# Performance work log

Measured on AMD Instinct MI355X. Metric: run time of the kernel, lower is better.

Reference implementation:

```python
import jax, jax.numpy as jnp
import numpy as np
from jax import lax

EPS = 1e-12  # F.normalize eps


def _normalize(x, axis):
    n = jnp.linalg.norm(x, axis=axis, keepdims=True)
    return x / jnp.maximum(n, EPS)


def setup_inputs() -> dict:
    key = jax.random.key(0)
    k1, k2 = jax.random.split(key)
    B, T, C, E = 4, 4096, 2048, 64
    return {
        "hidden_states": jax.random.normal(k1, (B, T, C), dtype=jnp.float32),
        "sim_matrix": jax.random.normal(k2, (C, E), dtype=jnp.float32),
        "gates": jnp.zeros((E,), dtype=jnp.float32),
        "temperature": jnp.ones((1,), dtype=jnp.float32),
        "experts_mask": jnp.ones((E,), dtype=jnp.float32),
        "min_experts_per_tok": 2,
    }


def reference(hidden_states, sim_matrix, gates, temperature, experts_mask, min_experts_per_tok):
    B, T, C = hidden_states.shape
    E = sim_matrix.shape[1]
    flat = hidden_states.reshape(B * T, C)  # (N, C)

    logit_scale = jax.nn.sigmoid(temperature)[0]
    # cosine-similarity style gating: row-normalized tokens x col-normalized sim matrix
    logits = _normalize(flat, axis=-1) @ _normalize(sim_matrix, axis=0)  # (N, E)
    logits = logits * experts_mask

    gated = jax.nn.relu(logits - gates * logit_scale)  # (N, E)
    hard = (gated > 0).astype(gated.dtype)
    # STE: forward = hard threshold, backward = identity on gated
    ste_mask = gated + lax.stop_gradient(hard - gated)

    # fallback: rows with no active expert get top-k(min_experts_per_tok) of logits
    inactive = jnp.sum(hard, axis=1) == 0  # (N,)
    _, topk_idx = lax.top_k(logits, min_experts_per_tok)  # (N, k)
    fallback = jnp.sum(jax.nn.one_hot(topk_idx, E, dtype=gated.dtype), axis=1)  # (N, E)

    activation_mask = jnp.where(inactive[:, None], fallback, ste_mask)
    return activation_mask, logits
```

## Files before the change

kernel.cpp:

```cpp
#include <hip/hip_runtime.h>
#include <cstdint>
#include <math.h>

#define N_TOK 16384
#define C_DIM 2048
#define E_DIM 64
#define TILE_T 64
#define KC 64
#define EPSN 1e-12f
#define NE ((size_t)N_TOK * E_DIM)

#define SCRATCH_FAST (6 * N_TOK * E_DIM + C_DIM * E_DIM + N_TOK + E_DIM)
#define SCRATCH_OLD (C_DIM * E_DIM + N_TOK + E_DIM)

__global__ __launch_bounds__(1024) void coln_kernel(const float* __restrict__ sim,
                                                    float* __restrict__ denc) {
    __shared__ float S[2][256 * 64];
    const int tid = threadIdx.x;
    {
        const float4* src = (const float4*)sim;
        float4* dst = (float4*)S[0];
        for (int i = tid; i < 4096; i += 1024) dst[i] = src[i];
    }
    __syncthreads();
    float acc = 0.f;
    for (int ch = 0; ch < 8; ++ch) {
        if (ch + 1 < 8) {
            const float4* src = (const float4*)(sim + (size_t)(ch + 1) * 256 * 64);
            float4* dst = (float4*)S[(ch + 1) & 1];
            for (int i = tid; i < 4096; i += 1024) dst[i] = src[i];
        }
        if (tid < 64) {
            const float* Sc = S[ch & 1];
#pragma unroll 8
            for (int r = 0; r < 256; ++r) {
                const float v = Sc[r * 64 + tid];
                acc = __fadd_rn(acc, __fmul_rn(v, v));
            }
        }
        __syncthreads();
    }
    if (tid < 64) denc[tid] = fmaxf(__fsqrt_rn(acc), EPSN);
}

__global__ __launch_bounds__(256) void bn_kernel(const float* __restrict__ sim,
                                                 const float* __restrict__ denc,
                                                 float* __restrict__ bnorm) {
    const int idx = blockIdx.x * 256 + threadIdx.x;
    const int e = idx & (E_DIM - 1);
    bnorm[idx] = __fdiv_rn(sim[idx], denc[e]);
}

__global__ __launch_bounds__(256) void tokn_kernel(const float* __restrict__ hs,
                                                   float* __restrict__ ntok) {
    const int t = blockIdx.x * 16 + (threadIdx.x >> 4);
    const int j = threadIdx.x & 15;
    const float4* p = (const float4*)(hs + (size_t)t * C_DIM + j * 128);
    float4 v0 = p[0], v1 = p[1];
    float r0 = __fmul_rn(v0.x, v0.x), r1 = __fmul_rn(v0.y, v0.y);
    float r2 = __fmul_rn(v0.z, v0.z), r3 = __fmul_rn(v0.w, v0.w);
    float r4 = __fmul_rn(v1.x, v1.x), r5 = __fmul_rn(v1.y, v1.y);
    float r6 = __fmul_rn(v1.z, v1.z), r7 = __fmul_rn(v1.w, v1.w);
#pragma unroll
    for (int i = 2; i < 32; i += 2) {
        float4 a = p[i], b = p[i + 1];
        r0 = __fadd_rn(r0, __fmul_rn(a.x, a.x));
        r1 = __fadd_rn(r1, __fmul_rn(a.y, a.y));
        r2 = __fadd_rn(r2, __fmul_rn(a.z, a.z));
        r3 = __fadd_rn(r3, __fmul_rn(a.w, a.w));
        r4 = __fadd_rn(r4, __fmul_rn(b.x, b.x));
        r5 = __fadd_rn(r5, __fmul_rn(b.y, b.y));
        r6 = __fadd_rn(r6, __fmul_rn(b.z, b.z));
        r7 = __fadd_rn(r7, __fmul_rn(b.w, b.w));
    }
    float leaf = __fadd_rn(__fadd_rn(__fadd_rn(r0, r1), __fadd_rn(r2, r3)),
                           __fadd_rn(__fadd_rn(r4, r5), __fadd_rn(r6, r7)));
    float v = leaf;
#pragma unroll
    for (int off = 1; off <= 8; off <<= 1)
        v = __fadd_rn(v, __shfl_xor(v, off, 64));
    if (j == 0) ntok[t] = fmaxf(__fsqrt_rn(v), EPSN);
}

__global__ __launch_bounds__(512) void logits_split_kernel(
        const float* __restrict__ hs, const float* __restrict__ bnorm,
        const float* __restrict__ ntok, float* __restrict__ parts) {
    __shared__ float As[TILE_T * 68];
    const int tid  = threadIdx.x;
    const int lane = tid & 63;
    const int w    = __builtin_amdgcn_readfirstlane(tid >> 6);
    const int tile = blockIdx.x * TILE_T;
    const int s    = blockIdx.y;
    const int cbeg = s * 6;
    const int cend = (cbeg + 6 < 32) ? cbeg + 6 : 32;

    const float4* hs4 = (const float4*)hs;
    const int tok0 = tid >> 4;
    const int tok1 = 32 + (tid >> 4);
    const int q    = tid & 15;
    const int rb0  = (tile + tok0) * (C_DIM / 4);
    const int rb1  = (tile + tok1) * (C_DIM / 4);
    const float dn0 = ntok[tile + tok0];
    const float dn1 = ntok[tile + tok1];

    float acc[8];
#pragma unroll
    for (int e = 0; e < 8; ++e) acc[e] = 0.f;

    float4 p0 = hs4[rb0 + cbeg * 16 + q];
    float4 p1 = hs4[rb1 + cbeg * 16 + q];

    for (int ch = cbeg; ch < cend; ++ch) {
        float4 n0, n1;
        n0.x = __fdiv_rn(p0.x, dn0); n0.y = __fdiv_rn(p0.y, dn0);
        n0.z = __fdiv_rn(p0.z, dn0); n0.w = __fdiv_rn(p0.w, dn0);
        n1.x = __fdiv_rn(p1.x, dn1); n1.y = __fdiv_rn(p1.y, dn1);
        n1.z = __fdiv_rn(p1.z, dn1); n1.w = __fdiv_rn(p1.w, dn1);
        *(float4*)&As[tok0 * 68 + 4 * q] = n0;
        *(float4*)&As[tok1 * 68 + 4 * q] = n1;
        __syncthreads();
        if (ch + 1 < cend) {
            p0 = hs4[rb0 + (ch + 1) * 16 + q];
            p1 = hs4[rb1 + (ch + 1) * 16 + q];
        }
        const int k0 = ch * KC;
#pragma unroll
        for (int k4 = 0; k4 < 16; ++k4) {
            const float4 a4 = *(const float4*)&As[lane * 68 + 4 * k4];
            const float* ac = (const float*)&a4;
            const float* Brow = bnorm + (size_t)(k0 + 4 * k4) * E_DIM + w * 8;
#pragma unroll
            for (int c = 0; c < 4; ++c) {
                const float a = ac[c];
#pragma unroll
                for (int e = 0; e < 8; ++e)
                    acc[e] = fmaf(a, Brow[c * E_DIM + e], acc[e]);
            }
        }
        __syncthreads();
    }

    float4* dst = (float4*)(parts + (size_t)s * NE +
                            (size_t)(tile + lane) * E_DIM + w * 8);
    dst[0] = make_float4(acc[0], acc[1], acc[2], acc[3]);
    dst[1] = make_float4(acc[4], acc[5], acc[6], acc[7]);
}

__global__ __launch_bounds__(256) void epilogue_kernel(
        const float* __restrict__ parts, const float* __restrict__ gates,
        const float* __restrict__ temp, const float* __restrict__ emask,
        const int* __restrict__ minkp, float* __restrict__ mask_out,
        float* __restrict__ logits_out) {
    const int lane = threadIdx.x & 63;
    const int wid  = blockIdx.x * (blockDim.x >> 6) + (threadIdx.x >> 6);
    const int nw   = gridDim.x * (blockDim.x >> 6);
    const float lscale = __fdiv_rn(1.f, __fadd_rn(1.f, expf(-temp[0])));
    const float g  = __fmul_rn(gates[lane], lscale);
    const float em = emask[lane];
    const int mk = *minkp;

    for (int t = wid; t < N_TOK; t += nw) {
        const size_t idx = (size_t)t * E_DIM + lane;
        float L = parts[idx];
#pragma unroll
        for (int s = 1; s < 6; ++s)
            L = __fadd_rn(L, parts[(size_t)s * NE + idx]);
        L = __fmul_rn(L, em);
        logits_out[idx] = L;

        const bool hard = (L - g) > 0.f;
        const unsigned long long act = __ballot(hard);
        float mv;
        if (act != 0ull) {
            mv = hard ? 1.f : 0.f;
        } else {
            unsigned long long chosen = 0ull;
            float Lc = L;
            for (int r = 0; r < mk; ++r) {
                float m = Lc;
                for (int o = 32; o > 0; o >>= 1) m = fmaxf(m, __shfl_xor(m, o, 64));
                const unsigned long long b = __ballot(Lc == m);
                const int ix = __ffsll((unsigned long long)b) - 1;
                chosen |= 1ull << ix;
                if (lane == ix) Lc = -INFINITY;
            }
            mv = ((chosen >> lane) & 1ull) ? 1.f : 0.f;
        }
        mask_out[idx] = mv;
    }
}

__global__ __launch_bounds__(512) void logits_kernel_old(
        const float* __restrict__ hs, const float* __restrict__ bnorm,
        const float* __restrict__ emask, const float* __restrict__ ntok,
        float* __restrict__ out_logits) {
    __shared__ float Al[KC * 65];
    const int tid  = threadIdx.x;
    const int lane = tid & 63;
    const int w    = __builtin_amdgcn_readfirstlane(tid >> 6);
    const int tile = blockIdx.x * TILE_T;
    const float4* hs4 = (const float4*)hs;
    const int tok0 = tid >> 4;
    const int tok1 = 32 + (tid >> 4);
    const int q    = tid & 15;
    const int rb0  = (tile + tok0) * (C_DIM / 4);
    const int rb1  = (tile + tok1) * (C_DIM / 4);
    const float dn0 = ntok[tile + tok0];
    const float dn1 = ntok[tile + tok1];
    float accT[8], accP[8];
#pragma unroll
    for (int e = 0; e < 8; ++e) { accT[e] = 0.f; accP[e] = 0.f; }
    float4 p0 = hs4[rb0 + q];
    float4 p1 = hs4[rb1 + q];
    for (int ch = 0; ch < C_DIM / KC; ++ch) {
        const int kb = 4 * q;
        Al[(kb + 0) * 65 + tok0] = __fdiv_rn(p0.x, dn0);
        Al[(kb + 1) * 65 + tok0] = __fdiv_rn(p0.y, dn0);
        Al[(kb + 2) * 65 + tok0] = __fdiv_rn(p0.z, dn0);
        Al[(kb + 3) * 65 + tok0] = __fdiv_rn(p0.w, dn0);
        Al[(kb + 0) * 65 + tok1] = __fdiv_rn(p1.x, dn1);
        Al[(kb + 1) * 65 + tok1] = __fdiv_rn(p1.y, dn1);
        Al[(kb + 2) * 65 + tok1] = __fdiv_rn(p1.z, dn1);
        Al[(kb + 3) * 65 + tok1] = __fdiv_rn(p1.w, dn1);
        __syncthreads();
        if (ch + 1 < C_DIM / KC) {
            p0 = hs4[rb0 + (ch + 1) * (KC / 4) + q];
            p1 = hs4[rb1 + (ch + 1) * (KC / 4) + q];
        }
        const int k0 = ch * KC;
#pragma unroll 4
        for (int k = 0; k < KC; ++k) {
            const float a = Al[k * 65 + lane];
            const float* Brow = bnorm + (size_t)(k0 + k) * E_DIM + w * 8;
#pragma unroll
            for (int e = 0; e < 8; ++e) accP[e] = fmaf(a, Brow[e], accP[e]);
        }
        __syncthreads();
        if ((ch + 1) % 6 == 0 || ch == C_DIM / KC - 1) {
#pragma unroll
            for (int e = 0; e < 8; ++e) {
                accT[e] = __fadd_rn(accT[e], accP[e]);
                accP[e] = 0.f;
            }
        }
    }
    float outv[8];
#pragma unroll
    for (int e = 0; e < 8; ++e)
        outv[e] = __fmul_rn(accT[e], emask[w * 8 + e]);
    float4* dst = (float4*)(out_logits + (size_t)(tile + lane) * E_DIM + w * 8);
    dst[0] = make_float4(outv[0], outv[1], outv[2], outv[3]);
    dst[1] = make_float4(outv[4], outv[5], outv[6], outv[7]);
}

__global__ __launch_bounds__(256) void mask_kernel_old(
        const float* __restrict__ logits, const float* __restrict__ gates,
        const float* __restrict__ temp, const int* __restrict__ minkp,
        float* __restrict__ mask_out) {
    const int lane = threadIdx.x & 63;
    const int wid  = blockIdx.x * (blockDim.x >> 6) + (threadIdx.x >> 6);
    const int nw   = gridDim.x * (blockDim.x >> 6);
    const float lscale = __fdiv_rn(1.f, __fadd_rn(1.f, expf(-temp[0])));
    const float g = __fmul_rn(gates[lane], lscale);
    const int mk = *minkp;
    for (int t = wid; t < N_TOK; t += nw) {
        const float L = logits[(size_t)t * E_DIM + lane];
        const bool hard = (L - g) > 0.f;
        const unsigned long long act = __ballot(hard);
        float mv;
        if (act != 0ull) {
            mv = hard ? 1.f : 0.f;
        } else {
            unsigned long long chosen = 0ull;
            float Lc = L;
            for (int r = 0; r < mk; ++r) {
                float m = Lc;
                for (int o = 32; o > 0; o >>= 1) m = fmaxf(m, __shfl_xor(m, o, 64));
                const unsigned long long b = __ballot(Lc == m);
                const int ix = __ffsll((unsigned long long)b) - 1;
                chosen |= 1ull << ix;
                if (lane == ix) Lc = -INFINITY;
            }
            mv = ((chosen >> lane) & 1ull) ? 1.f : 0.f;
        }
        mask_out[(size_t)t * E_DIM + lane] = mv;
    }
}

extern "C" void kernel_launch(void* const* d_in, const int* in_sizes, int n_in,
                              void* d_out, int out_size, void* d_ws, size_t ws_size,
                              hipStream_t stream) {
    const float* hs    = (const float*)d_in[0];
    const float* sim   = (const float*)d_in[1];
    const float* gates = (const float*)d_in[2];
    const float* temp  = (const float*)d_in[3];
    const float* emask = (const float*)d_in[4];
    const int*   mink  = (const int*)d_in[5];

    float* outm = (float*)d_out;
    float* outl = outm + NE;

    if (ws_size >= (size_t)SCRATCH_FAST * sizeof(float)) {
        float* parts = (float*)d_ws;
        float* bnorm = parts + 6 * NE;
        float* ntok  = bnorm + C_DIM * E_DIM;
        float* denc  = ntok + N_TOK;

        coln_kernel<<<1, 1024, 0, stream>>>(sim, denc);
        bn_kernel<<<(C_DIM * E_DIM) / 256, 256, 0, stream>>>(sim, denc, bnorm);
        tokn_kernel<<<N_TOK / 16, 256, 0, stream>>>(hs, ntok);
        logits_split_kernel<<<dim3(N_TOK / TILE_T, 6), 512, 0, stream>>>(
            hs, bnorm, ntok, parts);
        epilogue_kernel<<<1024, 256, 0, stream>>>(parts, gates, temp, emask,
                                                  mink, outm, outl);
    } else {
        float* scratch = (ws_size >= (size_t)SCRATCH_OLD * sizeof(float))
                             ? (float*)d_ws : outm;
        float* bnorm = scratch;
        float* ntok  = bnorm + C_DIM * E_DIM;
        float* denc  = ntok + N_TOK;
        coln_kernel<<<1, 1024, 0, stream>>>(sim, denc);
        bn_kernel<<<(C_DIM * E_DIM) / 256, 256, 0, stream>>>(sim, denc, bnorm);
        tokn_kernel<<<N_TOK / 16, 256, 0, stream>>>(hs, ntok);
        logits_kernel_old<<<N_TOK / TILE_T, 512, 0, stream>>>(hs, bnorm, emask,
                                                              ntok, outl);
        mask_kernel_old<<<512, 256, 0, stream>>>(outl, gates, temp, mink, outm);
    }
}
```

Baseline: 317.0 us.

## Stage token rows in LDS for norms and widen logits per-thread expert tile

The token-norm kernel now loads four token rows into shared memory with fully coalesced float4 reads, then reduces them with one wavefront per token. The split-K logits kernel drops from 512 to 256 threads per block. Each thread now accumulates 16 experts instead of 8 and loads four token rows per chunk, which halves the redundant LDS A-reads per FMA and doubles register reuse. The trade-off is higher register pressure and fewer threads available to hide latency, and the reduction order in the norm changes, which may alter rounding.

```diff
diff --git a/kernel.cpp b/kernel.cpp
--- a/kernel.cpp
+++ b/kernel.cpp
@@ -53,36 +53,42 @@
 
 __global__ __launch_bounds__(256) void tokn_kernel(const float* __restrict__ hs,
                                                    float* __restrict__ ntok) {
-    const int t = blockIdx.x * 16 + (threadIdx.x >> 4);
-    const int j = threadIdx.x & 15;
-    const float4* p = (const float4*)(hs + (size_t)t * C_DIM + j * 128);
-    float4 v0 = p[0], v1 = p[1];
-    float r0 = __fmul_rn(v0.x, v0.x), r1 = __fmul_rn(v0.y, v0.y);
-    float r2 = __fmul_rn(v0.z, v0.z), r3 = __fmul_rn(v0.w, v0.w);
-    float r4 = __fmul_rn(v1.x, v1.x), r5 = __fmul_rn(v1.y, v1.y);
-    float r6 = __fmul_rn(v1.z, v1.z), r7 = __fmul_rn(v1.w, v1.w);
-#pragma unroll
-    for (int i = 2; i < 32; i += 2) {
-        float4 a = p[i], b = p[i + 1];
-        r0 = __fadd_rn(r0, __fmul_rn(a.x, a.x));
-        r1 = __fadd_rn(r1, __fmul_rn(a.y, a.y));
-        r2 = __fadd_rn(r2, __fmul_rn(a.z, a.z));
-        r3 = __fadd_rn(r3, __fmul_rn(a.w, a.w));
-        r4 = __fadd_rn(r4, __fmul_rn(b.x, b.x));
-        r5 = __fadd_rn(r5, __fmul_rn(b.y, b.y));
-        r6 = __fadd_rn(r6, __fmul_rn(b.z, b.z));
-        r7 = __fadd_rn(r7, __fmul_rn(b.w, b.w));
-    }
-    float leaf = __fadd_rn(__fadd_rn(__fadd_rn(r0, r1), __fadd_rn(r2, r3)),
-                           __fadd_rn(__fadd_rn(r4, r5), __fadd_rn(r6, r7)));
-    float v = leaf;
-#pragma unroll
-    for (int off = 1; off <= 8; off <<= 1)
-        v = __fadd_rn(v, __shfl_xor(v, off, 64));
-    if (j == 0) ntok[t] = fmaxf(__fsqrt_rn(v), EPSN);
-}
-
-__global__ __launch_bounds__(512) void logits_split_kernel(
+    __shared__ float X[4 * 2112];
+    const int tid  = threadIdx.x;
+    const int tblk = blockIdx.x * 4;
+    const float4* src = (const float4*)(hs + (size_t)tblk * C_DIM);
+#pragma unroll
+    for (int it = 0; it < 8; ++it) {
+        const int g   = it * 256 + tid;
+        const float4 v = src[g];
+        const int tok = g >> 9;
+        const int f   = g & 511;
+        const int j   = f >> 5;
+        const int r4  = f & 31;
+        *(float4*)&X[tok * 2112 + j * 132 + r4 * 4] = v;
+    }
+    __syncthreads();
+    const int tok = tid >> 6;
+    const int j   = (tid >> 2) & 15;
+    const int qd  = tid & 3;
+    float ra = 0.f, rb = 0.f;
+#pragma unroll
+    for (int i = 0; i < 16; ++i) {
+        const float2 v = *(const float2*)&X[tok * 2112 + j * 132 + 8 * i + 2 * qd];
+        ra = __fadd_rn(ra, __fmul_rn(v.x, v.x));
+        rb = __fadd_rn(rb, __fmul_rn(v.y, v.y));
+    }
+    float v = __fadd_rn(ra, rb);
+    v = __fadd_rn(v, __shfl_xor(v, 1, 64));
+    v = __fadd_rn(v, __shfl_xor(v, 2, 64));
+    v = __fadd_rn(v, __shfl_xor(v, 4, 64));
+    v = __fadd_rn(v, __shfl_xor(v, 8, 64));
+    v = __fadd_rn(v, __shfl_xor(v, 16, 64));
+    v = __fadd_rn(v, __shfl_xor(v, 32, 64));
+    if ((tid & 63) == 0) ntok[tblk + tok] = fmaxf(__fsqrt_rn(v), EPSN);
+}
+
+__global__ __launch_bounds__(256) void logits_split_kernel(
         const float* __restrict__ hs, const float* __restrict__ bnorm,
         const float* __restrict__ ntok, float* __restrict__ parts) {
     __shared__ float As[TILE_T * 68];
@@ -95,45 +101,51 @@
     const int cend = (cbeg + 6 < 32) ? cbeg + 6 : 32;
 
     const float4* hs4 = (const float4*)hs;
-    const int tok0 = tid >> 4;
-    const int tok1 = 32 + (tid >> 4);
-    const int q    = tid & 15;
-    const int rb0  = (tile + tok0) * (C_DIM / 4);
-    const int rb1  = (tile + tok1) * (C_DIM / 4);
-    const float dn0 = ntok[tile + tok0];
-    const float dn1 = ntok[tile + tok1];
-
-    float acc[8];
-#pragma unroll
-    for (int e = 0; e < 8; ++e) acc[e] = 0.f;
-
-    float4 p0 = hs4[rb0 + cbeg * 16 + q];
-    float4 p1 = hs4[rb1 + cbeg * 16 + q];
+    const int q  = tid & 15;
+    const int r0 = tid >> 4;
+    int   rb[4];
+    float dn[4];
+#pragma unroll
+    for (int jj = 0; jj < 4; ++jj) {
+        rb[jj] = (tile + r0 + 16 * jj) * (C_DIM / 4);
+        dn[jj] = ntok[tile + r0 + 16 * jj];
+    }
+
+    float acc[16];
+#pragma unroll
+    for (int e = 0; e < 16; ++e) acc[e] = 0.f;
+
+    float4 p[4];
+#pragma unroll
+    for (int jj = 0; jj < 4; ++jj) p[jj] = hs4[rb[jj] + cbeg * 16 + q];
 
     for (int ch = cbeg; ch < cend; ++ch) {
-        float4 n0, n1;
-        n0.x = __fdiv_rn(p0.x, dn0); n0.y = __fdiv_rn(p0.y, dn0);
-        n0.z = __fdiv_rn(p0.z, dn0); n0.w = __fdiv_rn(p0.w, dn0);
-        n1.x = __fdiv_rn(p1.x, dn1); n1.y = __fdiv_rn(p1.y, dn1);
-        n1.z = __fdiv_rn(p1.z, dn1); n1.w = __fdiv_rn(p1.w, dn1);
-        *(float4*)&As[tok0 * 68 + 4 * q] = n0;
-        *(float4*)&As[tok1 * 68 + 4 * q] = n1;
+#pragma unroll
+        for (int jj = 0; jj < 4; ++jj) {
+            float4 n;
+            n.x = __fdiv_rn(p[jj].x, dn[jj]);
+            n.y = __fdiv_rn(p[jj].y, dn[jj]);
+            n.z = __fdiv_rn(p[jj].z, dn[jj]);
+            n.w = __fdiv_rn(p[jj].w, dn[jj]);
+            *(float4*)&As[(r0 + 16 * jj) * 68 + 4 * q] = n;
+        }
         __syncthreads();
         if (ch + 1 < cend) {
-            p0 = hs4[rb0 + (ch + 1) * 16 + q];
-            p1 = hs4[rb1 + (ch + 1) * 16 + q];
+#pragma unroll
+            for (int jj = 0; jj < 4; ++jj)
+                p[jj] = hs4[rb[jj] + (ch + 1) * 16 + q];
         }
         const int k0 = ch * KC;
 #pragma unroll
         for (int k4 = 0; k4 < 16; ++k4) {
             const float4 a4 = *(const float4*)&As[lane * 68 + 4 * k4];
             const float* ac = (const float*)&a4;
-            const float* Brow = bnorm + (size_t)(k0 + 4 * k4) * E_DIM + w * 8;
+            const float* Brow = bnorm + (size_t)(k0 + 4 * k4) * E_DIM + w * 16;
 #pragma unroll
             for (int c = 0; c < 4; ++c) {
                 const float a = ac[c];
 #pragma unroll
-                for (int e = 0; e < 8; ++e)
+                for (int e = 0; e < 16; ++e)
                     acc[e] = fmaf(a, Brow[c * E_DIM + e], acc[e]);
             }
         }
@@ -141,9 +153,11 @@
     }
 
     float4* dst = (float4*)(parts + (size_t)s * NE +
-                            (size_t)(tile + lane) * E_DIM + w * 8);
-    dst[0] = make_float4(acc[0], acc[1], acc[2], acc[3]);
-    dst[1] = make_float4(acc[4], acc[5], acc[6], acc[7]);
+                            (size_t)(tile + lane) * E_DIM + w * 16);
+    dst[0] = make_float4(acc[0],  acc[1],  acc[2],  acc[3]);
+    dst[1] = make_float4(acc[4],  acc[5],  acc[6],  acc[7]);
+    dst[2] = make_float4(acc[8],  acc[9],  acc[10], acc[11]);
+    dst[3] = make_float4(acc[12], acc[13], acc[14], acc[15]);
 }
 
 __global__ __launch_bounds__(256) void epilogue_kernel(
@@ -308,8 +322,8 @@
 
         coln_kernel<<<1, 1024, 0, stream>>>(sim, denc);
         bn_kernel<<<(C_DIM * E_DIM) / 256, 256, 0, stream>>>(sim, denc, bnorm);
-        tokn_kernel<<<N_TOK / 16, 256, 0, stream>>>(hs, ntok);
-        logits_split_kernel<<<dim3(N_TOK / TILE_T, 6), 512, 0, stream>>>(
+        tokn_kernel<<<N_TOK / 4, 256, 0, stream>>>(hs, ntok);
+        logits_split_kernel<<<dim3(N_TOK / TILE_T, 6), 256, 0, stream>>>(
             hs, bnorm, ntok, parts);
         epilogue_kernel<<<1024, 256, 0, stream>>>(parts, gates, temp, emask,
                                                   mink, outm, outl);
@@ -321,7 +335,7 @@
         float* denc  = ntok + N_TOK;
         coln_kernel<<<1, 1024, 0, stream>>>(sim, denc);
         bn_kernel<<<(C_DIM * E_DIM) / 256, 256, 0, stream>>>(sim, denc, bnorm);
-        tokn_kernel<<<N_TOK / 16, 256, 0, stream>>>(hs, ntok);
+        tokn_kernel<<<N_TOK / 4, 256, 0, stream>>>(hs, ntok);
         logits_kernel_old<<<N_TOK / TILE_T, 512, 0, stream>>>(hs, bnorm, emask,
                                                               ntok, outl);
         mask_kernel_old<<<512, 256, 0, stream>>>(outl, gates, temp, mink, outm);
```

Result: faster. 309.8 us (-2.3%).
